# Kernel optimization log

Measured on AMD Instinct MI355X. Metric: run time of the kernel, lower is better.

## Reference

```python
import jax, jax.numpy as jnp
import numpy as np

BN, T, D_MODEL = 128, 256, 128
D_INNER, D_STATE, D_CONV, DT_RANK = 2 * D_MODEL, 16, 4, 8  # mamba-ssm defaults


def silu(v):
    return v * jax.nn.sigmoid(v)


def setup_inputs() -> dict:
    key = jax.random.key(0)
    ks = jax.random.split(key, 8)
    s = 0.02
    A_log = jnp.log(jnp.tile(jnp.arange(1, D_STATE + 1, dtype=jnp.float32), (D_INNER, 1)))
    return {
        "x": jax.random.normal(ks[0], (BN, T, D_MODEL), jnp.float32),
        "in_proj_w": jax.random.normal(ks[1], (2 * D_INNER, D_MODEL), jnp.float32) * s,
        "conv_w": jax.random.normal(ks[2], (D_INNER, 1, D_CONV), jnp.float32) * s,
        "conv_b": jnp.zeros((D_INNER,), jnp.float32),
        "x_proj_w": jax.random.normal(ks[3], (DT_RANK + 2 * D_STATE, D_INNER), jnp.float32) * s,
        "dt_proj_w": jax.random.normal(ks[4], (D_INNER, DT_RANK), jnp.float32) * s,
        "dt_proj_b": jax.random.uniform(ks[5], (D_INNER,), jnp.float32, -4.0, -2.0),
        "A_log": A_log,
        "D": jnp.ones((D_INNER,), jnp.float32),
        "out_proj_w": jax.random.normal(ks[6], (D_MODEL, D_INNER), jnp.float32) * s,
        "down_w": jax.random.normal(ks[7], (D_MODEL, D_MODEL, 3), jnp.float32) * s,
        "down_b": jnp.zeros((D_MODEL,), jnp.float32),
        "ln_g": jnp.ones((D_MODEL,), jnp.float32),
        "ln_b": jnp.zeros((D_MODEL,), jnp.float32),
    }


def _mamba(x, in_proj_w, conv_w, conv_b, x_proj_w, dt_proj_w, dt_proj_b, A_log, D, out_proj_w):
    B = x.shape[0]
    xz = jnp.einsum('bld,ed->ble', x, in_proj_w)            # (B,L,2*di)
    xc, z = jnp.split(xz, 2, axis=-1)
    # depthwise causal conv over time
    xt = xc.transpose(0, 2, 1)                               # (B,di,L)
    xt = jax.lax.conv_general_dilated(xt, conv_w, (1,), [(D_CONV - 1, 0)],
                                      feature_group_count=D_INNER)
    xc = silu((xt + conv_b[None, :, None]).transpose(0, 2, 1))  # (B,L,di)
    x_dbl = jnp.einsum('bld,ed->ble', xc, x_proj_w)
    dt, Bm, Cm = jnp.split(x_dbl, [DT_RANK, DT_RANK + D_STATE], axis=-1)
    delta = jax.nn.softplus(jnp.einsum('blr,dr->bld', dt, dt_proj_w) + dt_proj_b)  # (B,L,di)
    A = -jnp.exp(A_log)                                       # (di,N)

    def step(h, inp):
        d_t, B_t, C_t, u_t = inp                              # (B,di),(B,N),(B,N),(B,di)
        dA = jnp.exp(d_t[..., None] * A)                      # (B,di,N)
        h = dA * h + (d_t * u_t)[..., None] * B_t[:, None, :]
        return h, jnp.einsum('bdn,bn->bd', h, C_t)

    h0 = jnp.zeros((B, D_INNER, D_STATE), x.dtype)
    _, ys = jax.lax.scan(step, h0, (delta.swapaxes(0, 1), Bm.swapaxes(0, 1),
                                    Cm.swapaxes(0, 1), xc.swapaxes(0, 1)))
    y = ys.swapaxes(0, 1) + xc * D                            # (B,L,di)
    y = y * silu(z)
    return jnp.einsum('ble,de->bld', y, out_proj_w)


def reference(x, in_proj_w, conv_w, conv_b, x_proj_w, dt_proj_w, dt_proj_b,
              A_log, D, out_proj_w, down_w, down_b, ln_g, ln_b):
    x_skip = x
    h = _mamba(x, in_proj_w, conv_w, conv_b, x_proj_w, dt_proj_w, dt_proj_b,
               A_log, D, out_proj_w)                          # dropout: eval mode = identity
    ht = h.transpose(0, 2, 1)                                 # (B,d,T)
    ht = jax.lax.conv_general_dilated(ht, down_w, (2,), [(1, 1)]) + down_b[None, :, None]
    h = ht.transpose(0, 2, 1)                                 # (B,T//2,d)
    mu = jnp.mean(h, axis=-1, keepdims=True)
    var = jnp.mean((h - mu) ** 2, axis=-1, keepdims=True)
    h = (h - mu) * jax.lax.rsqrt(var + 1e-5) * ln_g + ln_b
    return (h, x_skip)
```

## Files before the change

kernel.cpp:

```cpp
#include <hip/hip_runtime.h>
#include <hip/hip_bf16.h>


typedef __attribute__((ext_vector_type(8))) short bf16x8;
typedef __attribute__((ext_vector_type(4))) short bf16x4;
typedef __attribute__((ext_vector_type(4))) float f32x4;
using bf16 = __hip_bfloat16;

static __device__ __forceinline__ short f2s(float v) {
  union { bf16 b; short s; } u; u.b = (bf16)v; return u.s;
}
static __device__ __forceinline__ float s2f(short s) {
  union { short s; bf16 b; } u; u.s = s; return (float)u.b;
}

__global__ __launch_bounds__(256) void cvt_x(const float* __restrict__ x,
                                             short* __restrict__ xb,
                                             float* __restrict__ out1) {
  int i = (blockIdx.x * 256 + threadIdx.x) * 4;
  f32x4 v = *(const f32x4*)(x + i);
  bf16x4 o;
  o[0] = f2s(v[0]); o[1] = f2s(v[1]); o[2] = f2s(v[2]); o[3] = f2s(v[3]);
  *(bf16x4*)(xb + i) = o;
  *(f32x4*)(out1 + i) = v;
}

__global__ __launch_bounds__(256) void prep_w(const float* __restrict__ ipw,
                                              const float* __restrict__ xpw,
                                              short* __restrict__ ipwb,
                                              short* __restrict__ wxb) {
  int idx = blockIdx.x * 256 + threadIdx.x;
  if (idx < 65536) {
    ipwb[idx] = f2s(ipw[idx]);
  } else {
    int j = idx - 65536;
    int n = j >> 8;
    wxb[j] = (n < 40) ? f2s(xpw[j]) : (short)0;
  }
}

__global__ __launch_bounds__(256) void g_prep(const float* __restrict__ dwn,
                                              const float* __restrict__ opw,
                                              short* __restrict__ G) {
  const int k  = blockIdx.x >> 7;
  const int co = blockIdx.x & 127;
  const int e  = threadIdx.x;
  float acc = 0.f;
  for (int dm = 0; dm < 128; ++dm) {
    acc += dwn[(co * 128 + dm) * 3 + k] * opw[dm * 256 + e];
  }
  G[(size_t)(k * 128 + co) * 256 + e] = f2s(acc);
}

template<int N, int K, int MODE>
__global__ __launch_bounds__(256) void mgemm(const short* __restrict__ A,
                                             const short* __restrict__ W,
                                             float* __restrict__ C,
                                             short* __restrict__ xcpre,
                                             short* __restrict__ zact) {
  const int m_base = blockIdx.x * 64;
  const int n_base = blockIdx.y * 64;
  const int wave = threadIdx.x >> 6;
  const int lane = threadIdx.x & 63;
  const int r16  = lane & 15;
  const int quad = lane >> 4;
  f32x4 acc[4] = {};
  const short* Ap = A + (size_t)(m_base + wave * 16 + r16) * K + quad * 8;
  const short* Wp = W + (size_t)(n_base + r16) * K + quad * 8;
#pragma unroll
  for (int k0 = 0; k0 < K; k0 += 32) {
    bf16x8 a = *(const bf16x8*)(Ap + k0);
#pragma unroll
    for (int j = 0; j < 4; ++j) {
      bf16x8 b = *(const bf16x8*)(Wp + (size_t)j * 16 * K + k0);
      acc[j] = __builtin_amdgcn_mfma_f32_16x16x32_bf16(a, b, acc[j], 0, 0, 0);
    }
  }
#pragma unroll
  for (int j = 0; j < 4; ++j) {
    const int col = n_base + j * 16 + r16;
#pragma unroll
    for (int r = 0; r < 4; ++r) {
      const int row = m_base + wave * 16 + quad * 4 + r;
      if (MODE == 0) {
        C[(size_t)row * N + col] = acc[j][r];
      } else {
        if (col < 256) {
          xcpre[(size_t)row * 256 + col] = f2s(acc[j][r]);
        } else {
          float v = acc[j][r];
          zact[(size_t)row * 256 + (col - 256)] = f2s(v / (1.f + __expf(-v)));
        }
      }
    }
  }
}

__global__ __launch_bounds__(256) void mid_k(const short* __restrict__ xcpre,
                                             const float* __restrict__ cw,
                                             const float* __restrict__ cb,
                                             const short* __restrict__ wxb,
                                             const short* __restrict__ zact,
                                             const float* __restrict__ dtw,
                                             const float* __restrict__ dtb,
                                             short* __restrict__ xcT,
                                             short* __restrict__ dT,
                                             short* __restrict__ zT,
                                             float* __restrict__ SBC) {
  const int b  = blockIdx.x >> 2;
  const int t0 = (blockIdx.x & 3) * 64;
  const int tg = threadIdx.x >> 6;
  const int dl = threadIdx.x & 63;
  __shared__ short XC[64][264];
  __shared__ float DTL[64][8];
  const int tA = t0 + tg * 16;
#pragma unroll
  for (int dtile = 0; dtile < 4; ++dtile) {
    const int d = dtile * 64 + dl;
    const float w0 = cw[d * 4], w1 = cw[d * 4 + 1];
    const float w2 = cw[d * 4 + 2], w3 = cw[d * 4 + 3];
    const float bias = cb[d];
    const size_t base = (size_t)b * 65536 + d;
    float p0 = (tA >= 3) ? s2f(xcpre[base + (size_t)(tA - 3) * 256]) : 0.f;
    float p1 = (tA >= 2) ? s2f(xcpre[base + (size_t)(tA - 2) * 256]) : 0.f;
    float p2 = (tA >= 1) ? s2f(xcpre[base + (size_t)(tA - 1) * 256]) : 0.f;
    bf16x8 xr0, xr1, zr0, zr1;
#pragma unroll
    for (int i = 0; i < 16; ++i) {
      const int t = tA + i;
      float cur = s2f(xcpre[base + (size_t)t * 256]);
      float acc = bias + p0 * w0 + p1 * w1 + p2 * w2 + cur * w3;
      short s = f2s(acc / (1.f + __expf(-acc)));
      XC[tg * 16 + i][d] = s;
      short z = zact[base + (size_t)t * 256];
      if (i < 8) { xr0[i] = s; zr0[i] = z; } else { xr1[i - 8] = s; zr1[i - 8] = z; }
      p0 = p1; p1 = p2; p2 = cur;
    }
    const size_t ob = ((size_t)b * 256 + d) * 256 + tA;
    *(bf16x8*)(xcT + ob)     = xr0;
    *(bf16x8*)(xcT + ob + 8) = xr1;
    *(bf16x8*)(zT + ob)      = zr0;
    *(bf16x8*)(zT + ob + 8)  = zr1;
  }
  __syncthreads();
  {
    const int lane = threadIdx.x & 63;
    const int r16  = lane & 15;
    const int quad = lane >> 4;
    f32x4 acc[4] = {};
    const short* Wp = wxb + (size_t)r16 * 256 + quad * 8;
    const short* Xp = &XC[tg * 16 + r16][quad * 8];
#pragma unroll
    for (int k0 = 0; k0 < 256; k0 += 32) {
      bf16x8 a = *(const bf16x8*)(Xp + k0);
#pragma unroll
      for (int j = 0; j < 4; ++j) {
        bf16x8 bb = *(const bf16x8*)(Wp + (size_t)j * 16 * 256 + k0);
        acc[j] = __builtin_amdgcn_mfma_f32_16x16x32_bf16(a, bb, acc[j], 0, 0, 0);
      }
    }
#pragma unroll
    for (int j = 0; j < 3; ++j) {
      const int col = j * 16 + r16;
#pragma unroll
      for (int r = 0; r < 4; ++r) {
        const int tl = tg * 16 + quad * 4 + r;
        if (col < 8) {
          DTL[tl][col] = acc[j][r];
        } else if (col < 40) {
          SBC[((size_t)b * 256 + t0 + tl) * 32 + (col - 8)] = acc[j][r];
        }
      }
    }
  }
  __syncthreads();
#pragma unroll
  for (int dtile = 0; dtile < 4; ++dtile) {
    const int d = dtile * 64 + dl;
    float wd[8];
#pragma unroll
    for (int j = 0; j < 8; ++j) wd[j] = dtw[d * 8 + j];
    const float bd = dtb[d];
    bf16x8 dr0, dr1;
#pragma unroll
    for (int i = 0; i < 16; ++i) {
      const float* r = &DTL[tg * 16 + i][0];
      float acc = bd;
#pragma unroll
      for (int j = 0; j < 8; ++j) acc += r[j] * wd[j];
      const float delta = (acc > 20.f) ? acc : __logf(1.f + __expf(acc));
      short s = f2s(delta);
      if (i < 8) dr0[i] = s; else dr1[i - 8] = s;
    }
    const size_t ob = ((size_t)b * 256 + d) * 256 + tA;
    *(bf16x8*)(dT + ob)     = dr0;
    *(bf16x8*)(dT + ob + 8) = dr1;
  }
}

#define SC6_PREFETCH(BUF, CH) do {                                           \
    _Pragma("unroll")                                                        \
    for (int j_ = 0; j_ < 8; ++j_) {                                         \
      SBr[BUF][j_] = *(const f32x4*)(&S[(CH) * 8 + j_][q * 4]);              \
      SCr[BUF][j_] = *(const f32x4*)(&S[(CH) * 8 + j_][16 + q * 4]);         \
    }                                                                        \
    uu[BUF] = *(const bf16x8*)(xcT + tb + (CH) * 8);                         \
    dd[BUF] = *(const bf16x8*)(dT + tb + (CH) * 8);                          \
    if (q == 0) zz[BUF] = *(const bf16x8*)(zT + tb + (CH) * 8);              \
  } while (0)

#define SC6_COMPUTE(BUF, CH) do {                                            \
    _Pragma("unroll")                                                        \
    for (int tt_ = 0; tt_ < 8; ++tt_) {                                      \
      const int t_ = (CH) * 8 + tt_;                                         \
      const float delta_ = s2f(dd[BUF][tt_]);                                \
      const float u_ = s2f(uu[BUF][tt_]);                                    \
      const float du_ = delta_ * u_;                                         \
      const f32x4 Bq_ = SBr[BUF][tt_];                                       \
      const f32x4 Cq_ = SCr[BUF][tt_];                                       \
      float yt_ = 0.f;                                                       \
      _Pragma("unroll")                                                      \
      for (int n_ = 0; n_ < 4; ++n_) {                                       \
        const float dA_ = __builtin_amdgcn_exp2f(delta_ * A2[n_]);           \
        h[n_] = dA_ * h[n_] + du_ * Bq_[n_];                                 \
        yt_ += h[n_] * Cq_[n_];                                              \
      }                                                                      \
      yt_ += __shfl_xor(yt_, 1);                                             \
      yt_ += __shfl_xor(yt_, 2);                                             \
      if (q == 0)                                                            \
        yb[(rb + t_) * 256 + d] = f2s((yt_ + u_ * Dv) * s2f(zz[BUF][tt_]));  \
    }                                                                        \
  } while (0)

__global__ __launch_bounds__(128, 2) void scan6(const float* __restrict__ SBC,
                                                const short* __restrict__ xcT,
                                                const short* __restrict__ dT,
                                                const short* __restrict__ zT,
                                                const float* __restrict__ alog,
                                                const float* __restrict__ Dp,
                                                short* __restrict__ yb) {
  const int g = blockIdx.x & 7;
  const int b = blockIdx.x >> 3;
  const int q = threadIdx.x & 3;
  const int d = g * 32 + (threadIdx.x >> 2);
  const size_t rb = (size_t)b * 256;
  __shared__ float S[256][32];
  for (int i = threadIdx.x; i < 2048; i += 128) {
    *(f32x4*)(&S[i >> 3][(i & 7) * 4]) =
        *(const f32x4*)(SBC + (size_t)b * 8192 + i * 4);
  }
  float A2[4];
#pragma unroll
  for (int n = 0; n < 4; ++n)
    A2[n] = -__expf(alog[d * 16 + q * 4 + n]) * 1.44269504089f;
  const float Dv = Dp[d];
  float h[4] = {0.f, 0.f, 0.f, 0.f};
  const size_t tb = ((size_t)b * 256 + d) * 256;
  f32x4 SBr[2][8], SCr[2][8];
  bf16x8 uu[2], dd[2];
  bf16x8 zz[2] = {};
  uu[0] = *(const bf16x8*)(xcT + tb);
  dd[0] = *(const bf16x8*)(dT + tb);
  if (q == 0) zz[0] = *(const bf16x8*)(zT + tb);
  __syncthreads();
#pragma unroll
  for (int j_ = 0; j_ < 8; ++j_) {
    SBr[0][j_] = *(const f32x4*)(&S[j_][q * 4]);
    SCr[0][j_] = *(const f32x4*)(&S[j_][16 + q * 4]);
  }
  for (int c = 0; c < 32; c += 2) {
    SC6_PREFETCH(1, c + 1);
    SC6_COMPUTE(0, c);
    if (c + 2 < 32) SC6_PREFETCH(0, c + 2);
    SC6_COMPUTE(1, c + 1);
  }
}

__global__ __launch_bounds__(256) void od_k(const short* __restrict__ yb,
                                            const short* __restrict__ G,
                                            const float* __restrict__ db,
                                            const float* __restrict__ lng,
                                            const float* __restrict__ lnb,
                                            float* __restrict__ out) {
  const int wave = threadIdx.x >> 6;
  const int lane = threadIdx.x & 63;
  const int r16  = lane & 15;
  const int quad = lane >> 4;
  const int m_base = blockIdx.x * 64 + wave * 16;
  const int ma = m_base + r16;
  const int ba = ma >> 7, toa = ma & 127;
  f32x4 acc[8] = {};
  const bf16x8 az = {};
#pragma unroll
  for (int k = 0; k < 3; ++k) {
    const int tp = 2 * toa + k - 1;
    const bool valid = (tp >= 0) && (tp < 256);
    const int tpc = tp < 0 ? 0 : (tp > 255 ? 255 : tp);
    const short* Ap = yb + (size_t)(ba * 256 + tpc) * 256 + quad * 8;
    const short* Gp = G + (size_t)(k * 128 + r16) * 256 + quad * 8;
#pragma unroll
    for (int k0 = 0; k0 < 256; k0 += 32) {
      bf16x8 a = *(const bf16x8*)(Ap + k0);
      a = valid ? a : az;
#pragma unroll
      for (int j = 0; j < 8; ++j) {
        bf16x8 g = *(const bf16x8*)(Gp + (size_t)j * 16 * 256 + k0);
        acc[j] = __builtin_amdgcn_mfma_f32_16x16x32_bf16(a, g, acc[j], 0, 0, 0);
      }
    }
  }
  float dbv[8], g8[8], be8[8];
#pragma unroll
  for (int j = 0; j < 8; ++j) {
    const int col = j * 16 + r16;
    dbv[j] = db[col]; g8[j] = lng[col]; be8[j] = lnb[col];
  }
#pragma unroll
  for (int r = 0; r < 4; ++r) {
    float v[8];
    float s = 0.f;
#pragma unroll
    for (int j = 0; j < 8; ++j) { v[j] = acc[j][r] + dbv[j]; s += v[j]; }
    s += __shfl_xor(s, 1); s += __shfl_xor(s, 2);
    s += __shfl_xor(s, 4); s += __shfl_xor(s, 8);
    const float mu = s * (1.0f / 128.0f);
    float vs = 0.f;
#pragma unroll
    for (int j = 0; j < 8; ++j) { const float dd = v[j] - mu; vs += dd * dd; }
    vs += __shfl_xor(vs, 1); vs += __shfl_xor(vs, 2);
    vs += __shfl_xor(vs, 4); vs += __shfl_xor(vs, 8);
    const float rstd = rsqrtf(vs * (1.0f / 128.0f) + 1e-5f);
    const int rowm = m_base + quad * 4 + r;
#pragma unroll
    for (int j = 0; j < 8; ++j) {
      out[(size_t)rowm * 128 + j * 16 + r16] = (v[j] - mu) * rstd * g8[j] + be8[j];
    }
  }
}

static const size_t O_XCPRE = 0;
static const size_t O_XCT   = 16777216;
static const size_t O_ZACT  = 33554432;
static const size_t O_DT    = 50331648;
static const size_t O_SBC   = 67108864;
static const size_t O_XB    = 75497472;
static const size_t O_IPWB  = 92274688;

extern "C" void kernel_launch(void* const* d_in, const int* in_sizes, int n_in,
                              void* d_out, int out_size, void* d_ws, size_t ws_size,
                              hipStream_t stream) {
  const float* x    = (const float*)d_in[0];
  const float* ipw  = (const float*)d_in[1];
  const float* cw   = (const float*)d_in[2];
  const float* cb   = (const float*)d_in[3];
  const float* xpw  = (const float*)d_in[4];
  const float* dtw  = (const float*)d_in[5];
  const float* dtb  = (const float*)d_in[6];
  const float* alog = (const float*)d_in[7];
  const float* Dp   = (const float*)d_in[8];
  const float* opw  = (const float*)d_in[9];
  const float* dw   = (const float*)d_in[10];
  const float* db   = (const float*)d_in[11];
  const float* lng  = (const float*)d_in[12];
  const float* lnb  = (const float*)d_in[13];

  char*  ws     = (char*)d_ws;
  short* xcpre  = (short*)(ws + O_XCPRE);
  short* yb     = (short*)(ws + O_XCPRE);
  short* xcT    = (short*)(ws + O_XCT);
  short* zact   = (short*)(ws + O_ZACT);
  short* dT     = (short*)(ws + O_DT);
  float* SBC    = (float*)(ws + O_SBC);
  short* xb     = (short*)(ws + O_XB);
  short* zT     = (short*)(ws + O_XB);
  short* ipwb   = (short*)(ws + O_IPWB);
  short* G      = (short*)(ws + O_IPWB);
  float* out    = (float*)d_out;
  short* wxb    = (short*)out;
  float* out1   = out + 2097152;

  cvt_x<<<4096, 256, 0, stream>>>(x, xb, out1);
  prep_w<<<320, 256, 0, stream>>>(ipw, xpw, ipwb, wxb);
  mgemm<512, 128, 1><<<dim3(512, 8), 256, 0, stream>>>(
      xb, ipwb, nullptr, xcpre, zact);
  g_prep<<<384, 256, 0, stream>>>(dw, opw, G);
  mid_k<<<512, 256, 0, stream>>>(xcpre, cw, cb, wxb, zact, dtw, dtb,
                                 xcT, dT, zT, SBC);
  scan6<<<1024, 128, 0, stream>>>(SBC, xcT, dT, zT, alog, Dp, yb);
  od_k<<<256, 256, 0, stream>>>(yb, G, db, lng, lnb, out);
}
```

Measured before the change: 263.4 us.

## Transpose in-projection output via LDS and stream z directly to scan layout

The in-projection GEMM now transposes its tile through shared memory and writes xc-pre and silu(z) directly in (b,d,t) layout. This removes the z copy from mid_k and lets the conv read contiguous time vectors. mid_k is split into smaller 32-timestep blocks with twice the grid and the x_proj MFMA work redistributed over three waves. The cost is an extra LDS staging step and a barrier in the GEMM epilogue, plus redundant halo loads in mid_k.

```diff
diff --git a/kernel.cpp b/kernel.cpp
--- a/kernel.cpp
+++ b/kernel.cpp
@@ -52,12 +52,10 @@
   G[(size_t)(k * 128 + co) * 256 + e] = f2s(acc);
 }
 
-template<int N, int K, int MODE>
-__global__ __launch_bounds__(256) void mgemm(const short* __restrict__ A,
-                                             const short* __restrict__ W,
-                                             float* __restrict__ C,
-                                             short* __restrict__ xcpre,
-                                             short* __restrict__ zact) {
+__global__ __launch_bounds__(256) void inproj_k(const short* __restrict__ A,
+                                                const short* __restrict__ W,
+                                                short* __restrict__ xcpreT,
+                                                short* __restrict__ zTb) {
   const int m_base = blockIdx.x * 64;
   const int n_base = blockIdx.y * 64;
   const int wave = threadIdx.x >> 6;
@@ -65,111 +63,106 @@
   const int r16  = lane & 15;
   const int quad = lane >> 4;
   f32x4 acc[4] = {};
-  const short* Ap = A + (size_t)(m_base + wave * 16 + r16) * K + quad * 8;
-  const short* Wp = W + (size_t)(n_base + r16) * K + quad * 8;
-#pragma unroll
-  for (int k0 = 0; k0 < K; k0 += 32) {
+  const short* Ap = A + (size_t)(m_base + wave * 16 + r16) * 128 + quad * 8;
+  const short* Wp = W + (size_t)(n_base + r16) * 128 + quad * 8;
+#pragma unroll
+  for (int k0 = 0; k0 < 128; k0 += 32) {
     bf16x8 a = *(const bf16x8*)(Ap + k0);
 #pragma unroll
     for (int j = 0; j < 4; ++j) {
-      bf16x8 b = *(const bf16x8*)(Wp + (size_t)j * 16 * K + k0);
+      bf16x8 b = *(const bf16x8*)(Wp + (size_t)j * 16 * 128 + k0);
       acc[j] = __builtin_amdgcn_mfma_f32_16x16x32_bf16(a, b, acc[j], 0, 0, 0);
     }
   }
+  __shared__ short LT[64][72];
+  const bool isz = (n_base >= 256);
 #pragma unroll
   for (int j = 0; j < 4; ++j) {
-    const int col = n_base + j * 16 + r16;
 #pragma unroll
     for (int r = 0; r < 4; ++r) {
-      const int row = m_base + wave * 16 + quad * 4 + r;
-      if (MODE == 0) {
-        C[(size_t)row * N + col] = acc[j][r];
-      } else {
-        if (col < 256) {
-          xcpre[(size_t)row * 256 + col] = f2s(acc[j][r]);
-        } else {
-          float v = acc[j][r];
-          zact[(size_t)row * 256 + (col - 256)] = f2s(v / (1.f + __expf(-v)));
-        }
-      }
-    }
-  }
-}
-
-__global__ __launch_bounds__(256) void mid_k(const short* __restrict__ xcpre,
-                                             const float* __restrict__ cw,
-                                             const float* __restrict__ cb,
-                                             const short* __restrict__ wxb,
-                                             const short* __restrict__ zact,
-                                             const float* __restrict__ dtw,
-                                             const float* __restrict__ dtb,
-                                             short* __restrict__ xcT,
-                                             short* __restrict__ dT,
-                                             short* __restrict__ zT,
-                                             float* __restrict__ SBC) {
-  const int b  = blockIdx.x >> 2;
-  const int t0 = (blockIdx.x & 3) * 64;
+      float v = acc[j][r];
+      short s = isz ? f2s(v / (1.f + __expf(-v))) : f2s(v);
+      LT[j * 16 + r16][wave * 16 + quad * 4 + r] = s;
+    }
+  }
+  __syncthreads();
+  const int bb = m_base >> 8;
+  const int tbase = m_base & 255;
+  short* dst = isz ? zTb : xcpreT;
+  const int dbase = isz ? (n_base - 256) : n_base;
+#pragma unroll
+  for (int it = 0; it < 2; ++it) {
+    const int dw = (threadIdx.x >> 3) + it * 32;
+    const int tc = (threadIdx.x & 7) * 8;
+    bf16x8 v = *(const bf16x8*)(&LT[dw][tc]);
+    *(bf16x8*)(dst + (size_t)(bb * 256 + dbase + dw) * 256 + tbase + tc) = v;
+  }
+}
+
+__global__ __launch_bounds__(256, 4) void mid_k(const short* __restrict__ xcpreT,
+                                                const float* __restrict__ cw,
+                                                const float* __restrict__ cb,
+                                                const short* __restrict__ wxb,
+                                                const float* __restrict__ dtw,
+                                                const float* __restrict__ dtb,
+                                                short* __restrict__ xcT,
+                                                short* __restrict__ dT,
+                                                float* __restrict__ SBC) {
+  const int b  = blockIdx.x >> 3;
+  const int t0 = (blockIdx.x & 7) * 32;
   const int tg = threadIdx.x >> 6;
   const int dl = threadIdx.x & 63;
-  __shared__ short XC[64][264];
-  __shared__ float DTL[64][8];
-  const int tA = t0 + tg * 16;
+  const int tA = t0 + tg * 8;
+  __shared__ short XC[32][264];
+  __shared__ float DTL[32][8];
 #pragma unroll
   for (int dtile = 0; dtile < 4; ++dtile) {
     const int d = dtile * 64 + dl;
     const float w0 = cw[d * 4], w1 = cw[d * 4 + 1];
     const float w2 = cw[d * 4 + 2], w3 = cw[d * 4 + 3];
     const float bias = cb[d];
-    const size_t base = (size_t)b * 65536 + d;
-    float p0 = (tA >= 3) ? s2f(xcpre[base + (size_t)(tA - 3) * 256]) : 0.f;
-    float p1 = (tA >= 2) ? s2f(xcpre[base + (size_t)(tA - 2) * 256]) : 0.f;
-    float p2 = (tA >= 1) ? s2f(xcpre[base + (size_t)(tA - 1) * 256]) : 0.f;
-    bf16x8 xr0, xr1, zr0, zr1;
-#pragma unroll
-    for (int i = 0; i < 16; ++i) {
-      const int t = tA + i;
-      float cur = s2f(xcpre[base + (size_t)t * 256]);
-      float acc = bias + p0 * w0 + p1 * w1 + p2 * w2 + cur * w3;
-      short s = f2s(acc / (1.f + __expf(-acc)));
-      XC[tg * 16 + i][d] = s;
-      short z = zact[base + (size_t)t * 256];
-      if (i < 8) { xr0[i] = s; zr0[i] = z; } else { xr1[i - 8] = s; zr1[i - 8] = z; }
-      p0 = p1; p1 = p2; p2 = cur;
-    }
-    const size_t ob = ((size_t)b * 256 + d) * 256 + tA;
-    *(bf16x8*)(xcT + ob)     = xr0;
-    *(bf16x8*)(xcT + ob + 8) = xr1;
-    *(bf16x8*)(zT + ob)      = zr0;
-    *(bf16x8*)(zT + ob + 8)  = zr1;
+    const size_t base = ((size_t)b * 256 + d) * 256;
+    bf16x8 v = *(const bf16x8*)(xcpreT + base + tA);
+    bf16x8 hp = {};
+    if (tA >= 8) hp = *(const bf16x8*)(xcpreT + base + tA - 8);
+    float x3 = s2f(hp[5]), x2 = s2f(hp[6]), x1 = s2f(hp[7]);
+    bf16x8 outv;
+#pragma unroll
+    for (int i = 0; i < 8; ++i) {
+      const float cur = s2f(v[i]);
+      const float a = bias + x3 * w0 + x2 * w1 + x1 * w2 + cur * w3;
+      const short s = f2s(a / (1.f + __expf(-a)));
+      outv[i] = s;
+      XC[tg * 8 + i][d] = s;
+      x3 = x2; x2 = x1; x1 = cur;
+    }
+    *(bf16x8*)(xcT + base + tA) = outv;
   }
   __syncthreads();
-  {
-    const int lane = threadIdx.x & 63;
-    const int r16  = lane & 15;
-    const int quad = lane >> 4;
-    f32x4 acc[4] = {};
-    const short* Wp = wxb + (size_t)r16 * 256 + quad * 8;
-    const short* Xp = &XC[tg * 16 + r16][quad * 8];
+  if (tg < 3) {
+    const int r16  = dl & 15;
+    const int quad = dl >> 4;
+    f32x4 acc0 = {}, acc1 = {};
+    const short* Wp = wxb + (size_t)(tg * 16 + r16) * 256 + quad * 8;
 #pragma unroll
     for (int k0 = 0; k0 < 256; k0 += 32) {
-      bf16x8 a = *(const bf16x8*)(Xp + k0);
-#pragma unroll
-      for (int j = 0; j < 4; ++j) {
-        bf16x8 bb = *(const bf16x8*)(Wp + (size_t)j * 16 * 256 + k0);
-        acc[j] = __builtin_amdgcn_mfma_f32_16x16x32_bf16(a, bb, acc[j], 0, 0, 0);
-      }
-    }
-#pragma unroll
-    for (int j = 0; j < 3; ++j) {
-      const int col = j * 16 + r16;
-#pragma unroll
-      for (int r = 0; r < 4; ++r) {
-        const int tl = tg * 16 + quad * 4 + r;
-        if (col < 8) {
-          DTL[tl][col] = acc[j][r];
-        } else if (col < 40) {
-          SBC[((size_t)b * 256 + t0 + tl) * 32 + (col - 8)] = acc[j][r];
-        }
+      bf16x8 bb = *(const bf16x8*)(Wp + k0);
+      bf16x8 a0 = *(const bf16x8*)(&XC[r16][quad * 8 + k0]);
+      bf16x8 a1 = *(const bf16x8*)(&XC[16 + r16][quad * 8 + k0]);
+      acc0 = __builtin_amdgcn_mfma_f32_16x16x32_bf16(a0, bb, acc0, 0, 0, 0);
+      acc1 = __builtin_amdgcn_mfma_f32_16x16x32_bf16(a1, bb, acc1, 0, 0, 0);
+    }
+    const int col = tg * 16 + r16;
+#pragma unroll
+    for (int r = 0; r < 4; ++r) {
+      const int tl0 = quad * 4 + r;
+      const int tl1 = 16 + quad * 4 + r;
+      if (col < 8) {
+        DTL[tl0][col] = acc0[r];
+        DTL[tl1][col] = acc1[r];
+      } else if (col < 40) {
+        SBC[((size_t)b * 256 + t0 + tl0) * 32 + (col - 8)] = acc0[r];
+        SBC[((size_t)b * 256 + t0 + tl1) * 32 + (col - 8)] = acc1[r];
       }
     }
   }
@@ -181,20 +174,20 @@
 #pragma unroll
     for (int j = 0; j < 8; ++j) wd[j] = dtw[d * 8 + j];
     const float bd = dtb[d];
-    bf16x8 dr0, dr1;
-#pragma unroll
-    for (int i = 0; i < 16; ++i) {
-      const float* r = &DTL[tg * 16 + i][0];
+    const size_t base = ((size_t)b * 256 + d) * 256;
+    bf16x8 dv;
+#pragma unroll
+    for (int i = 0; i < 8; ++i) {
+      const int tl = tg * 8 + i;
+      const f32x4 p0 = *(const f32x4*)(&DTL[tl][0]);
+      const f32x4 p1 = *(const f32x4*)(&DTL[tl][4]);
       float acc = bd;
 #pragma unroll
-      for (int j = 0; j < 8; ++j) acc += r[j] * wd[j];
+      for (int j = 0; j < 4; ++j) acc += p0[j] * wd[j] + p1[j] * wd[4 + j];
       const float delta = (acc > 20.f) ? acc : __logf(1.f + __expf(acc));
-      short s = f2s(delta);
-      if (i < 8) dr0[i] = s; else dr1[i - 8] = s;
-    }
-    const size_t ob = ((size_t)b * 256 + d) * 256 + tA;
-    *(bf16x8*)(dT + ob)     = dr0;
-    *(bf16x8*)(dT + ob + 8) = dr1;
+      dv[i] = f2s(delta);
+    }
+    *(bf16x8*)(dT + base + tA) = dv;
   }
 }
 
@@ -340,7 +333,7 @@
 
 static const size_t O_XCPRE = 0;
 static const size_t O_XCT   = 16777216;
-static const size_t O_ZACT  = 33554432;
+static const size_t O_ZT    = 33554432;
 static const size_t O_DT    = 50331648;
 static const size_t O_SBC   = 67108864;
 static const size_t O_XB    = 75497472;
@@ -365,14 +358,13 @@
   const float* lnb  = (const float*)d_in[13];
 
   char*  ws     = (char*)d_ws;
-  short* xcpre  = (short*)(ws + O_XCPRE);
+  short* xcpreT = (short*)(ws + O_XCPRE);
   short* yb     = (short*)(ws + O_XCPRE);
   short* xcT    = (short*)(ws + O_XCT);
-  short* zact   = (short*)(ws + O_ZACT);
+  short* zT     = (short*)(ws + O_ZT);
   short* dT     = (short*)(ws + O_DT);
   float* SBC    = (float*)(ws + O_SBC);
   short* xb     = (short*)(ws + O_XB);
-  short* zT     = (short*)(ws + O_XB);
   short* ipwb   = (short*)(ws + O_IPWB);
   short* G      = (short*)(ws + O_IPWB);
   float* out    = (float*)d_out;
@@ -381,11 +373,10 @@
 
   cvt_x<<<4096, 256, 0, stream>>>(x, xb, out1);
   prep_w<<<320, 256, 0, stream>>>(ipw, xpw, ipwb, wxb);
-  mgemm<512, 128, 1><<<dim3(512, 8), 256, 0, stream>>>(
-      xb, ipwb, nullptr, xcpre, zact);
+  inproj_k<<<dim3(512, 8), 256, 0, stream>>>(xb, ipwb, xcpreT, zT);
   g_prep<<<384, 256, 0, stream>>>(dw, opw, G);
-  mid_k<<<512, 256, 0, stream>>>(xcpre, cw, cb, wxb, zact, dtw, dtb,
-                                 xcT, dT, zT, SBC);
+  mid_k<<<1024, 256, 0, stream>>>(xcpreT, cw, cb, wxb, dtw, dtb,
+                                  xcT, dT, SBC);
   scan6<<<1024, 128, 0, stream>>>(SBC, xcT, dT, zT, alog, Dp, yb);
   od_k<<<256, 256, 0, stream>>>(yb, G, db, lng, lnb, out);
 }
```

Result: faster. 256.0 us (-2.8%).
